# Kernel tuning notes

Hardware: AMD Instinct MI355X
Metric: run time of the kernel (lower is better)

The kernel has to match this reference:

```python
import jax, jax.numpy as jnp
import numpy as np

N_NODES = 200000
IN_SIZE = 128
OUT_SIZE = 128
N_EDGES = 600000


def setup_inputs() -> dict:
    key = jax.random.key(0)
    k1, k2, k3, k4 = jax.random.split(key, 4)
    embedding = jax.random.normal(k1, (N_NODES, IN_SIZE), dtype=jnp.float32)
    up2down_edge_index = jax.random.randint(k2, (2, N_EDGES), 0, N_NODES, dtype=jnp.int64)
    # GCNConv params (glorot weight, zero bias as in PyG defaults)
    scale = np.sqrt(6.0 / (IN_SIZE + OUT_SIZE)).astype(np.float32)
    W = jax.random.uniform(k3, (IN_SIZE, OUT_SIZE), dtype=jnp.float32, minval=-scale, maxval=scale)
    b = jnp.zeros((OUT_SIZE,), dtype=jnp.float32)
    return {"embedding": embedding, "up2down_edge_index": up2down_edge_index, "W": W, "b": b}


def reference(embedding, up2down_edge_index, W, b):
    # PyG GCNConv: add self-loops, symmetric normalization, linear transform,
    # scatter-sum aggregation, add bias.
    N = embedding.shape[0]
    loops = jnp.arange(N, dtype=up2down_edge_index.dtype)
    src = jnp.concatenate([up2down_edge_index[0], loops])  # message sources
    dst = jnp.concatenate([up2down_edge_index[1], loops])  # message targets

    # degree of each target node (edge_weight = 1)
    deg = jax.ops.segment_sum(jnp.ones_like(src, dtype=embedding.dtype), dst, num_segments=N)
    deg_inv_sqrt = jnp.where(deg > 0, jax.lax.rsqrt(jnp.maximum(deg, 1.0)), 0.0)
    norm = deg_inv_sqrt[src] * deg_inv_sqrt[dst]  # [E+N]

    h = embedding @ W  # [N, out]
    msg = h[src] * norm[:, None]  # gather + scale, [E+N, out]
    out = jax.ops.segment_sum(msg, dst, num_segments=N)  # scatter-add
    return out + b
```

## Files before the change

kernel.cpp:

```cpp
#include <hip/hip_runtime.h>
#include <hip/hip_bf16.h>
#include <stdint.h>

typedef __attribute__((ext_vector_type(8))) short short8v;
typedef __attribute__((ext_vector_type(4))) float f32x4;

__device__ __forceinline__ unsigned short f2bf(float f) {
  unsigned int u = __float_as_uint(f);
  u += 0x7fffu + ((u >> 16) & 1u);
  return (unsigned short)(u >> 16);
}
__device__ __forceinline__ unsigned int pack2bf(float a, float b) {
  return (unsigned int)f2bf(a) | ((unsigned int)f2bf(b) << 16);
}
__device__ __forceinline__ float bf_lo(unsigned int v) { return __uint_as_float(v << 16); }
__device__ __forceinline__ float bf_hi(unsigned int v) { return __uint_as_float(v & 0xffff0000u); }

__global__ void k_zero(uint4* __restrict__ p, int n16) {
  int i = blockIdx.x * blockDim.x + threadIdx.x;
  if (i < n16) {
    uint4 z; z.x = z.y = z.z = z.w = 0u;
    p[i] = z;
  }
}

__global__ void k_count(const int* __restrict__ dst, int* deg, int E) {
  int e = blockIdx.x * blockDim.x + threadIdx.x;
  if (e < E) atomicAdd(&deg[dst[e]], 1);
}

__global__ void k_blocksum(const int* __restrict__ deg, int* partials, float* dis, int N) {
  __shared__ int s[256];
  int t = threadIdx.x;
  int i = blockIdx.x * 256 + t;
  int c = (i < N) ? deg[i] : 0;
  if (i < N) dis[i] = rsqrtf((float)(c + 1));
  s[t] = c;
  __syncthreads();
  for (int off = 128; off > 0; off >>= 1) {
    if (t < off) s[t] += s[t + off];
    __syncthreads();
  }
  if (t == 0) partials[blockIdx.x] = s[0];
}

__global__ void k_scan_partials(int* partials, int nb) {
  __shared__ int s[1024];
  int t = threadIdx.x;
  s[t] = (t < nb) ? partials[t] : 0;
  __syncthreads();
  for (int off = 1; off < 1024; off <<= 1) {
    int v = (t >= off) ? s[t - off] : 0;
    __syncthreads();
    s[t] += v;
    __syncthreads();
  }
  if (t < nb) partials[t] = (t == 0) ? 0 : s[t - 1];
}

__global__ void k_scan_final(const int* __restrict__ deg, const int* __restrict__ partials,
                             int* csr_off, int N, int E) {
  __shared__ int s[256];
  int t = threadIdx.x;
  int i = blockIdx.x * 256 + t;
  int c = (i < N) ? deg[i] : 0;
  s[t] = c;
  __syncthreads();
  for (int off = 1; off < 256; off <<= 1) {
    int v = (t >= off) ? s[t - off] : 0;
    __syncthreads();
    s[t] += v;
    __syncthreads();
  }
  if (i < N) csr_off[i] = partials[blockIdx.x] + s[t] - c;
  if (i == 0) csr_off[N] = E;
}

__global__ void k_fill(const int* __restrict__ src, const int* __restrict__ dst,
                       const int* __restrict__ csr_off, int* cursor, int* csr_src, int E) {
  int e = blockIdx.x * blockDim.x + threadIdx.x;
  if (e < E) {
    int d = dst[e];
    int p = atomicAdd(&cursor[d], 1);
    csr_src[csr_off[d] + p] = src[e];
  }
}

__global__ void k_wprep(const float* __restrict__ W, unsigned short* __restrict__ Wfrag) {
  int t = blockIdx.x * 256 + threadIdx.x;
  int j = t & 7;
  int lane = (t >> 3) & 63;
  int ktct = t >> 9;
  int kt = ktct & 3, ct = ktct >> 2;
  int col = ct * 16 + (lane & 15);
  int k = kt * 32 + 4 * (lane >> 4) + (j & 3) + 16 * (j >> 2);
  Wfrag[t] = f2bf(W[k * 128 + col]);
}

__device__ __forceinline__ short8v pack8(float4 a, float4 b) {
  short8v r;
  r[0] = (short)f2bf(a.x); r[1] = (short)f2bf(a.y);
  r[2] = (short)f2bf(a.z); r[3] = (short)f2bf(a.w);
  r[4] = (short)f2bf(b.x); r[5] = (short)f2bf(b.y);
  r[6] = (short)f2bf(b.z); r[7] = (short)f2bf(b.w);
  return r;
}

__global__ __launch_bounds__(256) void k_gemm3(const float* __restrict__ X,
     const unsigned short* __restrict__ Wfrag, const float* __restrict__ dis,
     unsigned short* __restrict__ hs, int N) {
  __shared__ unsigned short Wl[16384];
  int t = threadIdx.x;
  #pragma unroll
  for (int q = 0; q < 8; ++q)
    ((uint4*)Wl)[q * 256 + t] = ((const uint4*)Wfrag)[q * 256 + t];
  __syncthreads();

  int wv = t >> 6, lane = t & 63;
  int lr = lane & 15, lg = lane >> 4;
  int row = blockIdx.x * 64 + wv * 16 + lr;

  short8v afr[4];
  if (row < N) {
    const float* xp = X + (size_t)row * 128 + 4 * lg;
    #pragma unroll
    for (int kt = 0; kt < 4; ++kt) {
      float4 v0 = *(const float4*)(xp + kt * 32);
      float4 v1 = *(const float4*)(xp + kt * 32 + 16);
      afr[kt] = pack8(v0, v1);
    }
  } else {
    #pragma unroll
    for (int kt = 0; kt < 4; ++kt) {
      float4 z = {0.f, 0.f, 0.f, 0.f};
      afr[kt] = pack8(z, z);
    }
  }
  float d = (row < N) ? dis[row] : 0.f;

  #pragma unroll
  for (int ct = 0; ct < 8; ++ct) {
    f32x4 acc = {0.f, 0.f, 0.f, 0.f};
    #pragma unroll
    for (int kt = 0; kt < 4; ++kt) {
      short8v wfr = *(const short8v*)(Wl + (((ct * 4 + kt) * 64 + lane) * 8));
      acc = __builtin_amdgcn_mfma_f32_16x16x32_bf16(wfr, afr[kt], acc, 0, 0, 0);
    }
    if (row < N) {
      uint2 uu;
      uu.x = pack2bf(acc[0] * d, acc[1] * d);
      uu.y = pack2bf(acc[2] * d, acc[3] * d);
      *(uint2*)(hs + (size_t)row * 128 + ct * 16 + 4 * lg) = uu;
    }
  }
}

__device__ __forceinline__ void acc8(float* a, uint4 g) {
  a[0] += bf_lo(g.x); a[1] += bf_hi(g.x);
  a[2] += bf_lo(g.y); a[3] += bf_hi(g.y);
  a[4] += bf_lo(g.z); a[5] += bf_hi(g.z);
  a[6] += bf_lo(g.w); a[7] += bf_hi(g.w);
}

__global__ __launch_bounds__(256) void k_agg2(const unsigned short* __restrict__ hs_,
     const int* __restrict__ csr_src, const int* __restrict__ csr_off,
     const float* __restrict__ dis, const float* __restrict__ bias,
     float* __restrict__ out, int N) {
  const uint4* hs = (const uint4*)hs_;
  int lane = threadIdx.x & 63;
  int c = lane & 15;
  int base = lane & 48;
  int gid = (blockIdx.x * blockDim.x + threadIdx.x) >> 4;
  int G = (gridDim.x * blockDim.x) >> 4;
  int i0 = (int)(((long long)gid * N) / G);
  int i1 = (int)(((long long)(gid + 1) * N) / G);
  if (i0 >= i1) return;
  float4 bA = ((const float4*)bias)[c * 2];
  float4 bB = ((const float4*)bias)[c * 2 + 1];
  int e1prev = csr_off[i0];
  for (int i = i0; i < i1; ++i) {
    int e0 = e1prev;
    int e1 = csr_off[i + 1];
    e1prev = e1;
    float a[8];
    uint4 sv = hs[(size_t)i * 16 + c];
    a[0] = bf_lo(sv.x); a[1] = bf_hi(sv.x);
    a[2] = bf_lo(sv.y); a[3] = bf_hi(sv.y);
    a[4] = bf_lo(sv.z); a[5] = bf_hi(sv.z);
    a[6] = bf_lo(sv.w); a[7] = bf_hi(sv.w);
    int e = e0;
    while (e < e1) {
      int p = e + c;
      int myidx = (p < e1) ? csr_src[p] : 0;
      int kb = (e1 - e < 16) ? (e1 - e) : 16;
      int k = 0;
      for (; k + 8 <= kb; k += 8) {
        int s[8];
        #pragma unroll
        for (int q = 0; q < 8; ++q) s[q] = __shfl(myidx, base + k + q);
        uint4 g[8];
        #pragma unroll
        for (int q = 0; q < 8; ++q) g[q] = hs[(size_t)s[q] * 16 + c];
        #pragma unroll
        for (int q = 0; q < 8; ++q) acc8(a, g[q]);
      }
      for (; k < kb; k += 4) {
        int s0 = __shfl(myidx, base + k);
        int s1 = __shfl(myidx, base + k + 1);
        int s2 = __shfl(myidx, base + k + 2);
        int s3 = __shfl(myidx, base + k + 3);
        bool v1 = (k + 1 < kb), v2 = (k + 2 < kb), v3 = (k + 3 < kb);
        uint4 g0 = hs[(size_t)s0 * 16 + c];
        uint4 g1 = hs[(size_t)(v1 ? s1 : i) * 16 + c];
        uint4 g2 = hs[(size_t)(v2 ? s2 : i) * 16 + c];
        uint4 g3 = hs[(size_t)(v3 ? s3 : i) * 16 + c];
        if (!v1) { g1.x = g1.y = g1.z = g1.w = 0u; }
        if (!v2) { g2.x = g2.y = g2.z = g2.w = 0u; }
        if (!v3) { g3.x = g3.y = g3.z = g3.w = 0u; }
        acc8(a, g0); acc8(a, g1); acc8(a, g2); acc8(a, g3);
      }
      e += kb;
    }
    float di = dis[i];
    float4 o0, o1;
    o0.x = fmaf(di, a[0], bA.x); o0.y = fmaf(di, a[1], bA.y);
    o0.z = fmaf(di, a[2], bA.z); o0.w = fmaf(di, a[3], bA.w);
    o1.x = fmaf(di, a[4], bB.x); o1.y = fmaf(di, a[5], bB.y);
    o1.z = fmaf(di, a[6], bB.z); o1.w = fmaf(di, a[7], bB.w);
    float4* op = (float4*)(out + (size_t)i * 128);
    op[c * 2] = o0;
    op[c * 2 + 1] = o1;
  }
}

extern "C" void kernel_launch(void* const* d_in, const int* in_sizes, int n_in,
                              void* d_out, int out_size, void* d_ws, size_t ws_size,
                              hipStream_t stream) {
  const float* X    = (const float*)d_in[0];
  const int*   edge = (const int*)d_in[1];
  const float* W    = (const float*)d_in[2];
  const float* bias = (const float*)d_in[3];
  float* out = (float*)d_out;
  int N = in_sizes[0] / 128;
  int E = in_sizes[1] / 2;
  const int* srcArr = edge;
  const int* dstArr = edge + E;

  char* w = (char*)d_ws;
  auto align = [](size_t x) { return (x + 255) & ~(size_t)255; };
  size_t o = 0;
  int*   deg      = (int*)(w + o);   o += align((size_t)N * 4);
  int*   cursor   = (int*)(w + o);   o += align((size_t)N * 4);
  float* dis      = (float*)(w + o); o += align((size_t)N * 4);
  int*   csr_off  = (int*)(w + o);   o += align(((size_t)N + 1) * 4);
  int*   csr_src  = (int*)(w + o);   o += align((size_t)E * 4);
  int*   partials = (int*)(w + o);   o += align((size_t)4096 * 4);
  unsigned short* Wfrag = (unsigned short*)(w + o); o += align((size_t)16384 * 2);
  unsigned short* hs    = (unsigned short*)(w + o);

  int nbN = (N + 255) / 256;
  int nbE = (E + 255) / 256;

  size_t zbytes = align((size_t)N * 4) + align((size_t)N * 4);
  int n16 = (int)(zbytes / 16);
  k_zero<<<(n16 + 255) / 256, 256, 0, stream>>>((uint4*)deg, n16);
  k_wprep<<<64, 256, 0, stream>>>(W, Wfrag);
  k_count<<<nbE, 256, 0, stream>>>(dstArr, deg, E);
  k_blocksum<<<nbN, 256, 0, stream>>>(deg, partials, dis, N);
  k_scan_partials<<<1, 1024, 0, stream>>>(partials, nbN);
  k_scan_final<<<nbN, 256, 0, stream>>>(deg, partials, csr_off, N, E);
  k_fill<<<nbE, 256, 0, stream>>>(srcArr, dstArr, csr_off, cursor, csr_src, E);
  k_gemm3<<<(N + 63) / 64, 256, 0, stream>>>(X, Wfrag, dis, hs, N);
  k_agg2<<<2048, 256, 0, stream>>>(hs, csr_src, csr_off, dis, bias, out, N);
}
```

Measured before the change: 163.2 us.

## Make GEMM blocks process several row chunks with register prefetch; merge prep kernels

The GEMM kernel now loops over four 64-row chunks per block. Each block loads W into LDS once and prefetches the next chunk's X rows into registers while the MFMAs for the current chunk run. The first X load is also issued before the LDS barrier, so it overlaps the W staging. Separately, the zeroing and W fragment prep kernels are merged into one launch. In exchange, the kernel needs more registers and launches fewer blocks, which can lower occupancy.

```diff
diff --git a/kernel.cpp b/kernel.cpp
--- a/kernel.cpp
+++ b/kernel.cpp
@@ -4,6 +4,8 @@
 
 typedef __attribute__((ext_vector_type(8))) short short8v;
 typedef __attribute__((ext_vector_type(4))) float f32x4;
+
+#define CPB 4
 
 __device__ __forceinline__ unsigned short f2bf(float f) {
   unsigned int u = __float_as_uint(f);
@@ -16,11 +18,24 @@
 __device__ __forceinline__ float bf_lo(unsigned int v) { return __uint_as_float(v << 16); }
 __device__ __forceinline__ float bf_hi(unsigned int v) { return __uint_as_float(v & 0xffff0000u); }
 
-__global__ void k_zero(uint4* __restrict__ p, int n16) {
-  int i = blockIdx.x * blockDim.x + threadIdx.x;
-  if (i < n16) {
-    uint4 z; z.x = z.y = z.z = z.w = 0u;
-    p[i] = z;
+__global__ void k_prep(uint4* __restrict__ zp, int n16,
+                       const float* __restrict__ W, unsigned short* __restrict__ Wfrag) {
+  int b = blockIdx.x;
+  if (b < 64) {
+    int t = b * 256 + threadIdx.x;
+    int j = t & 7;
+    int lane = (t >> 3) & 63;
+    int ktct = t >> 9;
+    int kt = ktct & 3, ct = ktct >> 2;
+    int col = ct * 16 + (lane & 15);
+    int k = kt * 32 + 4 * (lane >> 4) + (j & 3) + 16 * (j >> 2);
+    Wfrag[t] = f2bf(W[k * 128 + col]);
+  } else {
+    int i = (b - 64) * 256 + threadIdx.x;
+    if (i < n16) {
+      uint4 z; z.x = z.y = z.z = z.w = 0u;
+      zp[i] = z;
+    }
   }
 }
 
@@ -86,17 +101,6 @@
   }
 }
 
-__global__ void k_wprep(const float* __restrict__ W, unsigned short* __restrict__ Wfrag) {
-  int t = blockIdx.x * 256 + threadIdx.x;
-  int j = t & 7;
-  int lane = (t >> 3) & 63;
-  int ktct = t >> 9;
-  int kt = ktct & 3, ct = ktct >> 2;
-  int col = ct * 16 + (lane & 15);
-  int k = kt * 32 + 4 * (lane >> 4) + (j & 3) + 16 * (j >> 2);
-  Wfrag[t] = f2bf(W[k * 128 + col]);
-}
-
 __device__ __forceinline__ short8v pack8(float4 a, float4 b) {
   short8v r;
   r[0] = (short)f2bf(a.x); r[1] = (short)f2bf(a.y);
@@ -106,51 +110,84 @@
   return r;
 }
 
-__global__ __launch_bounds__(256) void k_gemm3(const float* __restrict__ X,
+__global__ __launch_bounds__(256) void k_gemm4(const float* __restrict__ X,
      const unsigned short* __restrict__ Wfrag, const float* __restrict__ dis,
-     unsigned short* __restrict__ hs, int N) {
+     unsigned short* __restrict__ hs, int N, int nch) {
   __shared__ unsigned short Wl[16384];
   int t = threadIdx.x;
   #pragma unroll
   for (int q = 0; q < 8; ++q)
     ((uint4*)Wl)[q * 256 + t] = ((const uint4*)Wfrag)[q * 256 + t];
-  __syncthreads();
 
   int wv = t >> 6, lane = t & 63;
   int lr = lane & 15, lg = lane >> 4;
-  int row = blockIdx.x * 64 + wv * 16 + lr;
-
-  short8v afr[4];
-  if (row < N) {
-    const float* xp = X + (size_t)row * 128 + 4 * lg;
+  int rowoff = wv * 16 + lr;
+  int chunk = blockIdx.x * CPB;
+
+  float4 xv[8];
+  float d = 0.f;
+  {
+    int row = chunk * 64 + rowoff;
+    if (chunk < nch && row < N) {
+      const float* xp = X + (size_t)row * 128 + 4 * lg;
+      #pragma unroll
+      for (int q = 0; q < 4; ++q) {
+        xv[2 * q]     = *(const float4*)(xp + q * 32);
+        xv[2 * q + 1] = *(const float4*)(xp + q * 32 + 16);
+      }
+      d = dis[row];
+    } else {
+      #pragma unroll
+      for (int q = 0; q < 8; ++q) { xv[q].x = xv[q].y = xv[q].z = xv[q].w = 0.f; }
+    }
+  }
+  __syncthreads();
+
+  for (int ci = 0; ci < CPB && chunk < nch; ++ci, ++chunk) {
+    float4 nxv[8];
+    float nd = 0.f;
+    bool hasnext = (ci + 1 < CPB) && (chunk + 1 < nch);
+    if (hasnext) {
+      int nrow = (chunk + 1) * 64 + rowoff;
+      if (nrow < N) {
+        const float* xp = X + (size_t)nrow * 128 + 4 * lg;
+        #pragma unroll
+        for (int q = 0; q < 4; ++q) {
+          nxv[2 * q]     = *(const float4*)(xp + q * 32);
+          nxv[2 * q + 1] = *(const float4*)(xp + q * 32 + 16);
+        }
+        nd = dis[nrow];
+      } else {
+        #pragma unroll
+        for (int q = 0; q < 8; ++q) { nxv[q].x = nxv[q].y = nxv[q].z = nxv[q].w = 0.f; }
+      }
+    }
+
+    short8v afr[4];
     #pragma unroll
-    for (int kt = 0; kt < 4; ++kt) {
-      float4 v0 = *(const float4*)(xp + kt * 32);
-      float4 v1 = *(const float4*)(xp + kt * 32 + 16);
-      afr[kt] = pack8(v0, v1);
-    }
-  } else {
+    for (int kt = 0; kt < 4; ++kt) afr[kt] = pack8(xv[2 * kt], xv[2 * kt + 1]);
+
+    int crow = chunk * 64 + rowoff;
     #pragma unroll
-    for (int kt = 0; kt < 4; ++kt) {
-      float4 z = {0.f, 0.f, 0.f, 0.f};
-      afr[kt] = pack8(z, z);
-    }
-  }
-  float d = (row < N) ? dis[row] : 0.f;
-
-  #pragma unroll
-  for (int ct = 0; ct < 8; ++ct) {
-    f32x4 acc = {0.f, 0.f, 0.f, 0.f};
-    #pragma unroll
-    for (int kt = 0; kt < 4; ++kt) {
-      short8v wfr = *(const short8v*)(Wl + (((ct * 4 + kt) * 64 + lane) * 8));
-      acc = __builtin_amdgcn_mfma_f32_16x16x32_bf16(wfr, afr[kt], acc, 0, 0, 0);
-    }
-    if (row < N) {
-      uint2 uu;
-      uu.x = pack2bf(acc[0] * d, acc[1] * d);
-      uu.y = pack2bf(acc[2] * d, acc[3] * d);
-      *(uint2*)(hs + (size_t)row * 128 + ct * 16 + 4 * lg) = uu;
+    for (int ct = 0; ct < 8; ++ct) {
+      f32x4 acc = {0.f, 0.f, 0.f, 0.f};
+      #pragma unroll
+      for (int kt = 0; kt < 4; ++kt) {
+        short8v wfr = *(const short8v*)(Wl + (((ct * 4 + kt) * 64 + lane) * 8));
+        acc = __builtin_amdgcn_mfma_f32_16x16x32_bf16(wfr, afr[kt], acc, 0, 0, 0);
+      }
+      if (crow < N) {
+        uint2 uu;
+        uu.x = pack2bf(acc[0] * d, acc[1] * d);
+        uu.y = pack2bf(acc[2] * d, acc[3] * d);
+        *(uint2*)(hs + (size_t)crow * 128 + ct * 16 + 4 * lg) = uu;
+      }
+    }
+
+    if (hasnext) {
+      #pragma unroll
+      for (int q = 0; q < 8; ++q) xv[q] = nxv[q];
+      d = nd;
     }
   }
 }
@@ -260,16 +297,16 @@
 
   int nbN = (N + 255) / 256;
   int nbE = (E + 255) / 256;
+  int nch = (N + 63) / 64;
 
   size_t zbytes = align((size_t)N * 4) + align((size_t)N * 4);
   int n16 = (int)(zbytes / 16);
-  k_zero<<<(n16 + 255) / 256, 256, 0, stream>>>((uint4*)deg, n16);
-  k_wprep<<<64, 256, 0, stream>>>(W, Wfrag);
+  k_prep<<<64 + (n16 + 255) / 256, 256, 0, stream>>>((uint4*)deg, n16, W, Wfrag);
   k_count<<<nbE, 256, 0, stream>>>(dstArr, deg, E);
   k_blocksum<<<nbN, 256, 0, stream>>>(deg, partials, dis, N);
   k_scan_partials<<<1, 1024, 0, stream>>>(partials, nbN);
   k_scan_final<<<nbN, 256, 0, stream>>>(deg, partials, csr_off, N, E);
   k_fill<<<nbE, 256, 0, stream>>>(srcArr, dstArr, csr_off, cursor, csr_src, E);
-  k_gemm3<<<(N + 63) / 64, 256, 0, stream>>>(X, Wfrag, dis, hs, N);
+  k_gemm4<<<(nch + CPB - 1) / CPB, 256, 0, stream>>>(X, Wfrag, dis, hs, N, nch);
   k_agg2<<<2048, 256, 0, stream>>>(hs, csr_src, csr_off, dis, bias, out, N);
 }
```

Result: no change. 165.6 us (+1.5%).
